# Performance work log

Measured on AMD Instinct MI355X. Metric: run time of the kernel, lower is better.

The kernel has to match this reference:

```python
import jax, jax.numpy as jnp
import numpy as np
import math

B, S, H, NH = 2, 2048, 1024, 16
HD = H // NH


def setup_inputs() -> dict:
    key = jax.random.key(0)
    k1, k2, k3 = jax.random.split(key, 3)
    hidden_states = jax.random.normal(k1, (B, S, H), dtype=jnp.float32)
    attention_mask = jnp.zeros((B, 1, 1, S), dtype=jnp.float32)
    w_qkv = jax.random.normal(k2, (3 * H, H), dtype=jnp.float32) * (1.0 / math.sqrt(H))
    w_out = jax.random.normal(k3, (H, H), dtype=jnp.float32) * (1.0 / math.sqrt(H))
    gate = jnp.ones((NH,), dtype=jnp.float32)
    return {"hidden_states": hidden_states, "attention_mask": attention_mask,
            "w_qkv": w_qkv, "w_out": w_out, "gate": gate}


def reference(hidden_states, attention_mask, w_qkv, w_out, gate):
    b, s, h = hidden_states.shape
    nh, hd = NH, HD
    # fused QKV projection (no bias)
    qkv = hidden_states @ w_qkv.T                      # [b, s, 3h]
    qkv = qkv.reshape(b, s, 3, nh, hd)
    q, k, v = jnp.moveaxis(qkv, 2, 0)                  # each [b, s, nh, hd]
    q = q.transpose(0, 2, 1, 3)                        # [b, nh, s, hd]
    k = k.transpose(0, 2, 1, 3)
    v = v.transpose(0, 2, 1, 3)
    scores = jnp.einsum('bhqd,bhkd->bhqk', q, k) / math.sqrt(hd)
    scores = scores + attention_mask                   # broadcast [b,1,1,s]
    probs = jax.nn.softmax(scores, axis=-1)            # dropout p=0 -> identity
    ctx = jnp.einsum('bhqk,bhkd->bhqd', probs, v)      # [b, nh, s, hd]
    ctx = ctx.transpose(0, 2, 1, 3)                    # [b, s, nh, hd]
    ctx = ctx * gate[None, None, :, None]              # per-head gating
    ctx = ctx.reshape(b, s, h)
    out = ctx @ w_out.T
    # all gates active (> 1e-4) -> active_gates/num_heads == 1, no rescale
    return out
```

## Files before the change

### kernel.cpp

```cpp
#include <hip/hip_runtime.h>
#include <stdint.h>


typedef __attribute__((ext_vector_type(8))) short short8;
typedef __attribute__((ext_vector_type(4))) float floatx4;
typedef __attribute__((ext_vector_type(4))) unsigned int uint4v;
typedef __attribute__((ext_vector_type(2))) unsigned int uint2v;

__device__ __forceinline__ unsigned short f2bf(float f) {
    unsigned int u = __float_as_uint(f);
    unsigned int r = u + 0x7fffu + ((u >> 16) & 1u);
    return (unsigned short)(r >> 16);
}
#if __has_builtin(__builtin_amdgcn_cvt_pk_bf16_f32)
__device__ __forceinline__ unsigned int pack_bf2(float lo, float hi) {
    auto v = __builtin_amdgcn_cvt_pk_bf16_f32(lo, hi);
    return __builtin_bit_cast(unsigned int, v);
}
#else
__device__ __forceinline__ unsigned int pack_bf2(float lo, float hi) {
    unsigned int a = __float_as_uint(lo) + 0x8000u;
    unsigned int b = __float_as_uint(hi) + 0x8000u;
    return __builtin_amdgcn_perm(b, a, 0x07060302u);
}
#endif

#if __has_builtin(__builtin_amdgcn_exp2f)
#define EXP2(x) __builtin_amdgcn_exp2f(x)
#else
#define EXP2(x) exp2f(x)
#endif

__device__ __forceinline__ void gl2lds16(const void* g, void* l) {
    __builtin_amdgcn_global_load_lds(
        (const __attribute__((address_space(1))) unsigned int*)g,
        (__attribute__((address_space(3))) unsigned int*)l, 16, 0, 0);
}

#define MFMA32(a, b, c) __builtin_amdgcn_mfma_f32_16x16x32_bf16((a), (b), (c), 0, 0, 0)

__global__ __launch_bounds__(256)
void cvt_all(const float* __restrict__ a, const float* __restrict__ b,
             const float* __restrict__ c, const float* __restrict__ mask,
             unsigned short* __restrict__ oa, unsigned short* __restrict__ ob,
             unsigned short* __restrict__ oc, float* __restrict__ m2b)
{
    int i = blockIdx.x * 256 + threadIdx.x;
    if (i >= 2097152) {
        int off = i - 2097152;
        float4 v = *(const float4*)(mask + (size_t)off * 4);
        const float L2E = 1.44269504f, C2 = -14.4269504f;
        float4 w;
        w.x = fmaf(v.x, L2E, C2); w.y = fmaf(v.y, L2E, C2);
        w.z = fmaf(v.z, L2E, C2); w.w = fmaf(v.w, L2E, C2);
        *(float4*)(m2b + (size_t)off * 4) = w;
        return;
    }
    const float* src; unsigned short* dst; int off;
    if (i < 1048576)      { src = a; dst = oa; off = i; }
    else if (i < 1835008) { src = b; dst = ob; off = i - 1048576; }
    else                  { src = c; dst = oc; off = i - 1835008; }
    float4 v = *(const float4*)(src + (size_t)off * 4);
    uint2v w;
    w[0] = pack_bf2(v.x, v.y);
    w[1] = pack_bf2(v.z, v.w);
    *(uint2v*)(dst + (size_t)off * 4) = w;
}

template<int MODE, int BN>
__global__ __launch_bounds__(256)
void gemm_nt(const unsigned short* __restrict__ A,
             const unsigned short* __restrict__ Bm,
             unsigned short* __restrict__ out0,
             unsigned short* __restrict__ out1,
             unsigned short* __restrict__ out2,
             float* __restrict__ outf,
             int N)
{
    constexpr int BUFB  = 8192 + BN * 64;
    constexpr int NSTEP = 32;
    constexpr int NA    = 2;
    constexpr int NB    = BN / 64;
    constexpr int BSL   = BN / 32;
    __shared__ unsigned char smem[3 * BUFB];
    const int K = 1024;
    const int tid  = threadIdx.x;
    const int wave = tid >> 6, lane = tid & 63;
    const int l15  = lane & 15, quad = lane >> 4;
    const int wm = wave >> 1, wn = wave & 1;

    int Lid = blockIdx.y * gridDim.x + blockIdx.x;
    int bm = (Lid & 7) * 4 + ((Lid >> 3) & 3);
    int bn = Lid >> 5;

    floatx4 acc[4][BSL];
#pragma unroll
    for (int i = 0; i < 4; i++)
#pragma unroll
        for (int j = 0; j < BSL; j++)
            acc[i][j] = floatx4{0.f, 0.f, 0.f, 0.f};

    int soffA[NA], soffB[NB];
#pragma unroll
    for (int l = 0; l < NA; l++) {
        int s = (wave * NA + l) * 64 + lane;
        int L = s >> 3, q = (s & 7) ^ (L & 7);
        soffA[l] = (L * 2 + (q >> 2)) * K + (q & 3) * 8;
    }
#pragma unroll
    for (int l = 0; l < NB; l++) {
        int s = (wave * NB + l) * 64 + lane;
        int L = s >> 3, q = (s & 7) ^ (L & 7);
        soffB[l] = (L * 2 + (q >> 2)) * K + (q & 3) * 8;
    }
    int aoff[4], boff[BSL];
#pragma unroll
    for (int i = 0; i < 4; i++) {
        int r = wm * 64 + i * 16 + l15, L = r >> 1;
        aoff[i] = L * 128 + (((((r & 1) << 2) | quad) ^ (L & 7)) * 16);
    }
#pragma unroll
    for (int j = 0; j < BSL; j++) {
        int r = wn * (BN / 2) + j * 16 + l15, L = r >> 1;
        boff[j] = 8192 + L * 128 + (((((r & 1) << 2) | quad) ^ (L & 7)) * 16);
    }

    const unsigned short* Abase = A  + (size_t)(bm * 128) * K;
    const unsigned short* Bbase = Bm + (size_t)(bn * BN) * K;

    auto STAGE = [&](int u, int bufb) {
        const int k0 = u * 32;
#pragma unroll
        for (int l = 0; l < NA; l++)
            gl2lds16(Abase + (size_t)soffA[l] + k0, &smem[bufb + (wave * NA + l) * 1024]);
#pragma unroll
        for (int l = 0; l < NB; l++)
            gl2lds16(Bbase + (size_t)soffB[l] + k0, &smem[bufb + 8192 + (wave * NB + l) * 1024]);
    };

    STAGE(0, 0);
    STAGE(1, BUFB);

    int b0 = 0, b2 = 2;
    for (int t = 0; t < NSTEP; t++) {
        asm volatile("" ::: "memory");
        __builtin_amdgcn_s_barrier();
        asm volatile("" ::: "memory");
        if (t + 2 < NSTEP) {
            STAGE(t + 2, b2 * BUFB);
            if (BN == 128) asm volatile("s_waitcnt vmcnt(8)" ::: "memory");
            else           asm volatile("s_waitcnt vmcnt(6)" ::: "memory");
        } else if (t + 2 == NSTEP) {
            if (BN == 128) asm volatile("s_waitcnt vmcnt(4)" ::: "memory");
            else           asm volatile("s_waitcnt vmcnt(3)" ::: "memory");
        } else {
            asm volatile("s_waitcnt vmcnt(0)" ::: "memory");
        }
        __builtin_amdgcn_s_barrier();
        asm volatile("" ::: "memory");

        const int cb = b0 * BUFB;
        short8 af[4], bfr[BSL];
#pragma unroll
        for (int i = 0; i < 4; i++)
            af[i] = *(const short8*)(&smem[cb + aoff[i]]);
#pragma unroll
        for (int j = 0; j < BSL; j++)
            bfr[j] = *(const short8*)(&smem[cb + boff[j]]);
#pragma unroll
        for (int i = 0; i < 4; i++)
#pragma unroll
            for (int j = 0; j < BSL; j++)
                acc[i][j] = MFMA32(af[i], bfr[j], acc[i][j]);

        b0 = (b0 == 2) ? 0 : b0 + 1;
        b2 = (b2 == 2) ? 0 : b2 + 1;
    }

#pragma unroll
    for (int i = 0; i < 4; i++) {
#pragma unroll
        for (int j = 0; j < BSL; j++) {
            int n = bn * BN + wn * (BN / 2) + j * 16 + l15;
#pragma unroll
            for (int r = 0; r < 4; r++) {
                int m = bm * 128 + wm * 64 + i * 16 + quad * 4 + r;
                float fv = acc[i][j][r];
                if (MODE == 1) {
                    outf[(size_t)m * N + n] = fv;
                } else {
                    int t = n >> 10;
                    int h = (n >> 6) & 15;
                    int d = n & 63;
                    int b = m >> 11, si = m & 2047;
                    if (t == 2) {
                        int sip = (si & ~31) | (((si >> 2) & 3) << 3)
                                | (((si >> 4) & 1) << 2) | (si & 3);
                        out2[(((size_t)(b * 16 + h)) * 64 + d) * 2048 + sip] = f2bf(fv);
                    } else {
                        if (t == 0) fv *= 0.18033688f;
                        size_t off = (((size_t)(b * 16 + h)) * 2048 + si) * 64 + d;
                        unsigned short* dst = (t == 0) ? out0 : out1;
                        dst[off] = f2bf(fv);
                    }
                }
            }
        }
    }
}

__global__ __launch_bounds__(256, 4)
void attn_kernel(const unsigned short* __restrict__ Qb,
                 const unsigned short* __restrict__ Kb,
                 const unsigned short* __restrict__ VbT,
                 const float* __restrict__ m2b,
                 const float* __restrict__ gateb,
                 unsigned short* __restrict__ ctx)
{
    __shared__ unsigned char smem[16384];
    const int S = 2048;
    const int tid  = threadIdx.x;
    const int wave = tid >> 6, lane = tid & 63;
    const int l15  = lane & 15, quad = lane >> 4;

    int Lid = blockIdx.y * gridDim.x + blockIdx.x;
    int bh = (Lid & 7) * 4 + ((Lid >> 3) & 3);
    int qc = Lid >> 5;
    const int b = bh >> 4, h = bh & 15;
    const int q0 = qc * 64 + wave * 16;

    const size_t headoff = (size_t)bh * S * 64;
    const unsigned short* Qh  = Qb  + headoff;
    const unsigned short* Kh  = Kb  + headoff;
    const unsigned short* VhT = VbT + headoff;
    const float* m2p = m2b + (size_t)b * S;

    int koff, voff;
    {
        int s = wave * 64 + lane;
        int key = s >> 3;
        koff = key * 64 + (((s & 7) ^ (key & 7)) * 8);
        int d = s >> 2;
        voff = d * 2048 + (((s & 3) ^ (d & 3)) * 8);
    }
    int qkoff[2];
#pragma unroll
    for (int s2 = 0; s2 < 2; s2++)
        qkoff[s2] = l15 * 128 + (((s2 * 4 + quad) ^ (l15 & 7)) * 16);
    const int pvoff = 4096 + l15 * 64 + ((quad ^ (l15 & 3)) * 16);

    short8 aq[2];
#pragma unroll
    for (int s2 = 0; s2 < 2; s2++)
        aq[s2] = *(const short8*)(Qh + (size_t)(q0 + l15) * 64 + s2 * 32 + quad * 8);

    floatx4 o[4];
    floatx4 lq = floatx4{0.f, 0.f, 0.f, 0.f};
#pragma unroll
    for (int dt = 0; dt < 4; dt++) o[dt] = floatx4{0.f, 0.f, 0.f, 0.f};

    const uint4v onesu = {0x3F803F80u, 0x3F803F80u, 0x3F803F80u, 0x3F803F80u};
    const short8 ONES = __builtin_bit_cast(short8, onesu);

    gl2lds16(Kh + koff, &smem[wave * 1024]);
    gl2lds16(VhT + voff, &smem[4096 + wave * 1024]);

    for (int i = 0; i < 64; i++) {
        const int cb = (i & 1) * 8192;
        const int nb = ((i + 1) & 1) * 8192;
        const int kb = i * 32;
        floatx4 mf[2];
#pragma unroll
        for (int t = 0; t < 2; t++)
            mf[t] = *(const floatx4*)(m2p + kb + t * 16 + quad * 4);
        asm volatile("" ::: "memory");
        __builtin_amdgcn_s_barrier();
        asm volatile("" ::: "memory");
        if (i + 1 < 64) {
            const int kbn = (i + 1) * 32;
            gl2lds16(Kh + (size_t)kbn * 64 + koff, &smem[nb + wave * 1024]);
            gl2lds16(VhT + kbn + voff, &smem[nb + 4096 + wave * 1024]);
            asm volatile("s_waitcnt vmcnt(2)" ::: "memory");
        } else {
            asm volatile("s_waitcnt vmcnt(0)" ::: "memory");
        }
        __builtin_amdgcn_s_barrier();
        asm volatile("" ::: "memory");

        short8 kf[2][2];
#pragma unroll
        for (int t = 0; t < 2; t++)
#pragma unroll
            for (int s2 = 0; s2 < 2; s2++)
                kf[t][s2] = *(const short8*)(&smem[cb + qkoff[s2] + t * 2048]);
        short8 vf[4];
#pragma unroll
        for (int dt = 0; dt < 4; dt++)
            vf[dt] = *(const short8*)(&smem[cb + pvoff + dt * 1024]);

        floatx4 st0 = MFMA32(kf[0][0], aq[0], mf[0]);
        floatx4 st1 = MFMA32(kf[1][0], aq[0], mf[1]);
        st0 = MFMA32(kf[0][1], aq[1], st0);
        st1 = MFMA32(kf[1][1], aq[1], st1);
        float e00 = EXP2(st0[0]), e01 = EXP2(st0[1]);
        float e02 = EXP2(st0[2]), e03 = EXP2(st0[3]);
        float e10 = EXP2(st1[0]), e11 = EXP2(st1[1]);
        float e12 = EXP2(st1[2]), e13 = EXP2(st1[3]);
        uint4v pu = {pack_bf2(e00, e01), pack_bf2(e02, e03),
                     pack_bf2(e10, e11), pack_bf2(e12, e13)};
        short8 pf = __builtin_bit_cast(short8, pu);
#pragma unroll
        for (int dt = 0; dt < 4; dt++)
            o[dt] = MFMA32(vf[dt], pf, o[dt]);
        lq = MFMA32(ONES, pf, lq);
    }

    float iv = gateb[h] / lq[0];
    size_t base = ((size_t)(b * 2048 + q0 + l15)) * 1024 + h * 64 + quad * 4;
#pragma unroll
    for (int dt = 0; dt < 4; dt++) {
        uint2v w;
        w[0] = pack_bf2(o[dt][0] * iv, o[dt][1] * iv);
        w[1] = pack_bf2(o[dt][2] * iv, o[dt][3] * iv);
        *(uint2v*)(ctx + base + dt * 16) = w;
    }
}

extern "C" void kernel_launch(void* const* d_in, const int* in_sizes, int n_in,
                              void* d_out, int out_size, void* d_ws, size_t ws_size,
                              hipStream_t stream)
{
    const float* hidden = (const float*)d_in[0];
    const float* mask   = (const float*)d_in[1];
    const float* w_qkv  = (const float*)d_in[2];
    const float* w_out  = (const float*)d_in[3];
    const float* gate   = (const float*)d_in[4];
    float* out = (float*)d_out;

    unsigned short* q_buf = (unsigned short*)d_ws;
    unsigned short* k_buf = q_buf + 4194304;
    unsigned short* v_buf = k_buf + 4194304;
    unsigned short* c_buf = v_buf + 4194304;
    unsigned short* h_bf  = c_buf + 4194304;
    unsigned short* wq_bf = h_bf  + 4194304;
    unsigned short* wo_bf = wq_bf + 3145728;
    float* m2_buf = (float*)(wo_bf + 1048576);

    cvt_all<<<8196, 256, 0, stream>>>(hidden, w_qkv, w_out, mask,
                                      h_bf, wq_bf, wo_bf, m2_buf);

    gemm_nt<0, 128><<<dim3(24, 32), 256, 0, stream>>>(h_bf, wq_bf, q_buf, k_buf, v_buf, nullptr, 3072);
    attn_kernel<<<dim3(32, 32), 256, 0, stream>>>(q_buf, k_buf, v_buf, m2_buf, gate, c_buf);
    gemm_nt<1, 64><<<dim3(16, 32), 256, 0, stream>>>(c_buf, wo_bf, nullptr, nullptr, nullptr, out, 1024);
}
```

Measured before the change: 191.3 us.

## Process two 16-query subtiles per wave in attention to reuse K/V fragments

Each attention wave now handles 32 query rows as two 16-row subtiles that share the same K and V fragments read from LDS, so each block covers 128 queries and the grid is halved. The V tile's shared-memory layout and swizzle are changed to match the new fragment read pattern. The goal is to cut LDS reads and global K/V traffic per query. In exchange the kernel holds twice the accumulators and Q fragments (launch bounds lowered to 2), and there are half as many blocks, which reduces occupancy and latency hiding.

```diff
diff --git a/kernel.cpp b/kernel.cpp
--- a/kernel.cpp
+++ b/kernel.cpp
@@ -209,7 +209,7 @@
     }
 }
 
-__global__ __launch_bounds__(256, 4)
+__global__ __launch_bounds__(256, 2)
 void attn_kernel(const unsigned short* __restrict__ Qb,
                  const unsigned short* __restrict__ Kb,
                  const unsigned short* __restrict__ VbT,
@@ -227,7 +227,7 @@
     int bh = (Lid & 7) * 4 + ((Lid >> 3) & 3);
     int qc = Lid >> 5;
     const int b = bh >> 4, h = bh & 15;
-    const int q0 = qc * 64 + wave * 16;
+    const int q0 = qc * 128 + wave * 32;
 
     const size_t headoff = (size_t)bh * S * 64;
     const unsigned short* Qh  = Qb  + headoff;
@@ -240,24 +240,31 @@
         int s = wave * 64 + lane;
         int key = s >> 3;
         koff = key * 64 + (((s & 7) ^ (key & 7)) * 8);
-        int d = s >> 2;
-        voff = d * 2048 + (((s & 3) ^ (d & 3)) * 8);
+        int L = s >> 3, q = (s & 7) ^ (L & 7);
+        voff = (L * 2 + (q >> 2)) * 2048 + (q & 3) * 8;
     }
     int qkoff[2];
 #pragma unroll
     for (int s2 = 0; s2 < 2; s2++)
         qkoff[s2] = l15 * 128 + (((s2 * 4 + quad) ^ (l15 & 7)) * 16);
-    const int pvoff = 4096 + l15 * 64 + ((quad ^ (l15 & 3)) * 16);
-
-    short8 aq[2];
-#pragma unroll
-    for (int s2 = 0; s2 < 2; s2++)
-        aq[s2] = *(const short8*)(Qh + (size_t)(q0 + l15) * 64 + s2 * 32 + quad * 8);
-
-    floatx4 o[4];
-    floatx4 lq = floatx4{0.f, 0.f, 0.f, 0.f};
-#pragma unroll
-    for (int dt = 0; dt < 4; dt++) o[dt] = floatx4{0.f, 0.f, 0.f, 0.f};
+    const int pvoff = 4096 + (l15 >> 1) * 128
+                    + (((((l15 & 1) << 2) | quad) ^ ((l15 >> 1) & 7)) * 16);
+
+    short8 aq[2][2];
+#pragma unroll
+    for (int sub = 0; sub < 2; sub++)
+#pragma unroll
+        for (int s2 = 0; s2 < 2; s2++)
+            aq[sub][s2] = *(const short8*)(Qh + (size_t)(q0 + sub * 16 + l15) * 64 + s2 * 32 + quad * 8);
+
+    floatx4 o[2][4];
+    floatx4 lq[2];
+#pragma unroll
+    for (int sub = 0; sub < 2; sub++) {
+        lq[sub] = floatx4{0.f, 0.f, 0.f, 0.f};
+#pragma unroll
+        for (int dt = 0; dt < 4; dt++) o[sub][dt] = floatx4{0.f, 0.f, 0.f, 0.f};
+    }
 
     const uint4v onesu = {0x3F803F80u, 0x3F803F80u, 0x3F803F80u, 0x3F803F80u};
     const short8 ONES = __builtin_bit_cast(short8, onesu);
@@ -298,31 +305,38 @@
         for (int dt = 0; dt < 4; dt++)
             vf[dt] = *(const short8*)(&smem[cb + pvoff + dt * 1024]);
 
-        floatx4 st0 = MFMA32(kf[0][0], aq[0], mf[0]);
-        floatx4 st1 = MFMA32(kf[1][0], aq[0], mf[1]);
-        st0 = MFMA32(kf[0][1], aq[1], st0);
-        st1 = MFMA32(kf[1][1], aq[1], st1);
-        float e00 = EXP2(st0[0]), e01 = EXP2(st0[1]);
-        float e02 = EXP2(st0[2]), e03 = EXP2(st0[3]);
-        float e10 = EXP2(st1[0]), e11 = EXP2(st1[1]);
-        float e12 = EXP2(st1[2]), e13 = EXP2(st1[3]);
-        uint4v pu = {pack_bf2(e00, e01), pack_bf2(e02, e03),
-                     pack_bf2(e10, e11), pack_bf2(e12, e13)};
-        short8 pf = __builtin_bit_cast(short8, pu);
-#pragma unroll
-        for (int dt = 0; dt < 4; dt++)
-            o[dt] = MFMA32(vf[dt], pf, o[dt]);
-        lq = MFMA32(ONES, pf, lq);
-    }
-
-    float iv = gateb[h] / lq[0];
-    size_t base = ((size_t)(b * 2048 + q0 + l15)) * 1024 + h * 64 + quad * 4;
-#pragma unroll
-    for (int dt = 0; dt < 4; dt++) {
-        uint2v w;
-        w[0] = pack_bf2(o[dt][0] * iv, o[dt][1] * iv);
-        w[1] = pack_bf2(o[dt][2] * iv, o[dt][3] * iv);
-        *(uint2v*)(ctx + base + dt * 16) = w;
+#pragma unroll
+        for (int sub = 0; sub < 2; sub++) {
+            floatx4 st0 = MFMA32(kf[0][0], aq[sub][0], mf[0]);
+            floatx4 st1 = MFMA32(kf[1][0], aq[sub][0], mf[1]);
+            st0 = MFMA32(kf[0][1], aq[sub][1], st0);
+            st1 = MFMA32(kf[1][1], aq[sub][1], st1);
+            float e00 = EXP2(st0[0]), e01 = EXP2(st0[1]);
+            float e02 = EXP2(st0[2]), e03 = EXP2(st0[3]);
+            float e10 = EXP2(st1[0]), e11 = EXP2(st1[1]);
+            float e12 = EXP2(st1[2]), e13 = EXP2(st1[3]);
+            uint4v pu = {pack_bf2(e00, e01), pack_bf2(e02, e03),
+                         pack_bf2(e10, e11), pack_bf2(e12, e13)};
+            short8 pf = __builtin_bit_cast(short8, pu);
+#pragma unroll
+            for (int dt = 0; dt < 4; dt++)
+                o[sub][dt] = MFMA32(vf[dt], pf, o[sub][dt]);
+            lq[sub] = MFMA32(ONES, pf, lq[sub]);
+        }
+    }
+
+    float g = gateb[h];
+#pragma unroll
+    for (int sub = 0; sub < 2; sub++) {
+        float iv = g / lq[sub][0];
+        size_t base = ((size_t)(b * 2048 + q0 + sub * 16 + l15)) * 1024 + h * 64 + quad * 4;
+#pragma unroll
+        for (int dt = 0; dt < 4; dt++) {
+            uint2v w;
+            w[0] = pack_bf2(o[sub][dt][0] * iv, o[sub][dt][1] * iv);
+            w[1] = pack_bf2(o[sub][dt][2] * iv, o[sub][dt][3] * iv);
+            *(uint2v*)(ctx + base + dt * 16) = w;
+        }
     }
 }
 
@@ -350,6 +364,6 @@
                                       h_bf, wq_bf, wo_bf, m2_buf);
 
     gemm_nt<0, 128><<<dim3(24, 32), 256, 0, stream>>>(h_bf, wq_bf, q_buf, k_buf, v_buf, nullptr, 3072);
-    attn_kernel<<<dim3(32, 32), 256, 0, stream>>>(q_buf, k_buf, v_buf, m2_buf, gate, c_buf);
+    attn_kernel<<<dim3(16, 32), 256, 0, stream>>>(q_buf, k_buf, v_buf, m2_buf, gate, c_buf);
     gemm_nt<1, 64><<<dim3(16, 32), 256, 0, stream>>>(c_buf, wo_bf, nullptr, nullptr, nullptr, out, 1024);
 }
```

Result: no change. 188.3 us (-1.5%).

## Software-pipeline attention loop: overlap QK MFMA with previous tile's exp/PV

Applied to the files above, without the earlier changes.

Restructures the attention inner loop so each iteration computes the QK scores for the current key block while applying exp and the PV MFMAs to the previous block's scores and V fragments, with a prologue of dummy zeros and an epilogue for the last block. It also changes the V^T shared-memory swizzle layout and the matching read offsets. The aim is to hide exp/MFMA dependency latency by interleaving independent work. In exchange it carries extra live registers (previous scores and V fragments), which could lower occupancy.

```diff
diff --git a/kernel.cpp b/kernel.cpp
--- a/kernel.cpp
+++ b/kernel.cpp
@@ -240,14 +240,15 @@
         int s = wave * 64 + lane;
         int key = s >> 3;
         koff = key * 64 + (((s & 7) ^ (key & 7)) * 8);
-        int d = s >> 2;
-        voff = d * 2048 + (((s & 3) ^ (d & 3)) * 8);
+        int L = s >> 3, q = (s & 7) ^ (L & 7);
+        voff = (L * 2 + (q >> 2)) * 2048 + (q & 3) * 8;
     }
     int qkoff[2];
 #pragma unroll
     for (int s2 = 0; s2 < 2; s2++)
         qkoff[s2] = l15 * 128 + (((s2 * 4 + quad) ^ (l15 & 7)) * 16);
-    const int pvoff = 4096 + l15 * 64 + ((quad ^ (l15 & 3)) * 16);
+    const int pvoff = 4096 + (l15 >> 1) * 128
+                    + (((((l15 & 1) << 2) | quad) ^ ((l15 >> 1) & 7)) * 16);
 
     short8 aq[2];
 #pragma unroll
@@ -261,6 +262,13 @@
 
     const uint4v onesu = {0x3F803F80u, 0x3F803F80u, 0x3F803F80u, 0x3F803F80u};
     const short8 ONES = __builtin_bit_cast(short8, onesu);
+    const short8 ZERO8 = __builtin_bit_cast(short8, uint4v{0u, 0u, 0u, 0u});
+
+    floatx4 st0p = floatx4{-1e30f, -1e30f, -1e30f, -1e30f};
+    floatx4 st1p = st0p;
+    short8 vfp[4];
+#pragma unroll
+    for (int dt = 0; dt < 4; dt++) vfp[dt] = ZERO8;
 
     gl2lds16(Kh + koff, &smem[wave * 1024]);
     gl2lds16(VhT + voff, &smem[4096 + wave * 1024]);
@@ -293,25 +301,44 @@
 #pragma unroll
             for (int s2 = 0; s2 < 2; s2++)
                 kf[t][s2] = *(const short8*)(&smem[cb + qkoff[s2] + t * 2048]);
-        short8 vf[4];
+        short8 vfc[4];
 #pragma unroll
         for (int dt = 0; dt < 4; dt++)
-            vf[dt] = *(const short8*)(&smem[cb + pvoff + dt * 1024]);
-
-        floatx4 st0 = MFMA32(kf[0][0], aq[0], mf[0]);
-        floatx4 st1 = MFMA32(kf[1][0], aq[0], mf[1]);
-        st0 = MFMA32(kf[0][1], aq[1], st0);
-        st1 = MFMA32(kf[1][1], aq[1], st1);
-        float e00 = EXP2(st0[0]), e01 = EXP2(st0[1]);
-        float e02 = EXP2(st0[2]), e03 = EXP2(st0[3]);
-        float e10 = EXP2(st1[0]), e11 = EXP2(st1[1]);
-        float e12 = EXP2(st1[2]), e13 = EXP2(st1[3]);
+            vfc[dt] = *(const short8*)(&smem[cb + pvoff + dt * 1024]);
+
+        floatx4 st0c = MFMA32(kf[0][0], aq[0], mf[0]);
+        floatx4 st1c = MFMA32(kf[1][0], aq[0], mf[1]);
+        st0c = MFMA32(kf[0][1], aq[1], st0c);
+        st1c = MFMA32(kf[1][1], aq[1], st1c);
+
+        float e00 = EXP2(st0p[0]), e01 = EXP2(st0p[1]);
+        float e02 = EXP2(st0p[2]), e03 = EXP2(st0p[3]);
+        float e10 = EXP2(st1p[0]), e11 = EXP2(st1p[1]);
+        float e12 = EXP2(st1p[2]), e13 = EXP2(st1p[3]);
         uint4v pu = {pack_bf2(e00, e01), pack_bf2(e02, e03),
                      pack_bf2(e10, e11), pack_bf2(e12, e13)};
         short8 pf = __builtin_bit_cast(short8, pu);
 #pragma unroll
         for (int dt = 0; dt < 4; dt++)
-            o[dt] = MFMA32(vf[dt], pf, o[dt]);
+            o[dt] = MFMA32(vfp[dt], pf, o[dt]);
+        lq = MFMA32(ONES, pf, lq);
+
+        st0p = st0c; st1p = st1c;
+#pragma unroll
+        for (int dt = 0; dt < 4; dt++) vfp[dt] = vfc[dt];
+    }
+
+    {
+        float e00 = EXP2(st0p[0]), e01 = EXP2(st0p[1]);
+        float e02 = EXP2(st0p[2]), e03 = EXP2(st0p[3]);
+        float e10 = EXP2(st1p[0]), e11 = EXP2(st1p[1]);
+        float e12 = EXP2(st1p[2]), e13 = EXP2(st1p[3]);
+        uint4v pu = {pack_bf2(e00, e01), pack_bf2(e02, e03),
+                     pack_bf2(e10, e11), pack_bf2(e12, e13)};
+        short8 pf = __builtin_bit_cast(short8, pu);
+#pragma unroll
+        for (int dt = 0; dt < 4; dt++)
+            o[dt] = MFMA32(vfp[dt], pf, o[dt]);
         lq = MFMA32(ONES, pf, lq);
     }
 
```

After: 194.1 us. Within noise of the previous version (+1.5%).
